# Optimization experiments

Hardware: AMD Instinct MI355X
Metric: run time of the kernel (lower is better)

The kernel has to match this reference:

```python
import jax, jax.numpy as jnp
import numpy as np


def _neighbor_sum(x_pad):
    """3x3 box filter with zero center (8-neighbor sum), VALID conv on a padded input."""
    k = jnp.array([[1., 1., 1.], [1., 0., 1.], [1., 1., 1.]], dtype=x_pad.dtype)
    k = k.reshape(1, 1, 3, 3)  # OIHW
    return jax.lax.conv_general_dilated(
        x_pad, k, window_strides=(1, 1), padding='VALID',
        dimension_numbers=('NCHW', 'OIHW', 'NCHW'))


def setup_inputs() -> dict:
    key = jax.random.key(0)
    k1, k2 = jax.random.split(key)
    B, C, H, W = 1, 1, 4096, 4096
    out_image = jax.random.uniform(k1, (B, C, H, W), dtype=jnp.float32)      # predicted probabilities
    segment_image = jax.random.uniform(k2, (B, C, H, W), dtype=jnp.float32)  # target map
    return {"out_image": out_image, "segment_image": segment_image}


def reference(out_image, segment_image):
    pad = ((0, 0), (0, 0), (1, 1), (1, 1))
    out_pad = jnp.pad(out_image, pad)          # constant 0 pad, as F.pad(..., value=0)
    seg_pad = jnp.pad(segment_image, pad)
    out_rev_pad = 1.0 - out_pad                # reverse AFTER padding: border becomes 1

    sig_seg_1 = 9.0 - _neighbor_sum(seg_pad)       # [B,C,H,W]
    sig_out_0 = 9.0 - _neighbor_sum(out_rev_pad)   # [B,C,H,W]

    W1 = jnp.squeeze(sig_seg_1)   # [H,W] for B=C=1
    M0 = jnp.squeeze(sig_out_0)
    seg = jnp.squeeze(segment_image)
    out = jnp.squeeze(out_image)

    eps = 1e-5
    loss = -(W1 * seg * jnp.log(out + eps) + M0 * (1.0 - seg) * jnp.log(1.0 - out + eps))
    return loss.mean()
```

## Files before the change

kernel.cpp:

```cpp
#include <hip/hip_runtime.h>

#define H 4096
#define W 4096
#define R 8
#define TC 4
#define TPB 256
#define STRIP (TPB*TC)
#define NSTRIP (W/STRIP)
#define NBAND (H/R)
#define NBLK (NSTRIP*NBAND)
#define LN2 0.69314718055994531f

template<bool INTERIOR>
__device__ __forceinline__ float band_loss(const float* __restrict__ sp0,
                                           const float* __restrict__ op0,
                                           int r0, bool lv, bool rv) {
  float sa[TC], sb[TC], sc[TC];
  float oa[TC], ob[TC], oc[TC];
  float sLa, sLb, sLc, sRa, sRb, sRc;
  float oLa, oLb, oLc, oRa, oRb, oRc;

  const float* sp = sp0 - W;
  const float* op = op0 - W;

  auto loadrow = [&](bool valid, float* sv, float* ov,
                     float& sl, float& sr, float& ol, float& orr) {
    if (valid) {
      const float4 fs = *reinterpret_cast<const float4*>(sp);
      const float4 fo = *reinterpret_cast<const float4*>(op);
      sv[0] = fs.x; sv[1] = fs.y; sv[2] = fs.z; sv[3] = fs.w;
      ov[0] = fo.x; ov[1] = fo.y; ov[2] = fo.z; ov[3] = fo.w;
      sl  = lv ? sp[-1] : 0.f;
      ol  = lv ? op[-1] : 0.f;
      sr  = rv ? sp[TC] : 0.f;
      orr = rv ? op[TC] : 0.f;
    } else {
      sv[0] = sv[1] = sv[2] = sv[3] = 0.f;
      ov[0] = ov[1] = ov[2] = ov[3] = 0.f;
      sl = sr = ol = orr = 0.f;
    }
  };

  loadrow(INTERIOR || (r0 - 1 >= 0), sa, oa, sLa, sRa, oLa, oRa);
  sp += W; op += W;
  loadrow(true, sb, ob, sLb, sRb, oLb, oRb);

  float acc = 0.f;

  #pragma unroll
  for (int i = 0; i < R; ++i) {
    sp += W; op += W;
    loadrow(INTERIOR || (r0 + i + 1 < H), sc, oc, sLc, sRc, oLc, oRc);

    float cs[TC], co[TC];
    #pragma unroll
    for (int k = 0; k < TC; ++k) {
      cs[k] = sa[k] + sb[k] + sc[k];
      co[k] = oa[k] + ob[k] + oc[k];
    }
    const float csL = sLa + sLb + sLc;
    const float csR = sRa + sRb + sRc;
    const float coL = oLa + oLb + oLc;
    const float coR = oRa + oRb + oRc;

    #pragma unroll
    for (int k = 0; k < TC; ++k) {
      const float cl  = (k == 0)    ? csL : cs[k-1];
      const float cr  = (k == TC-1) ? csR : cs[k+1];
      const float nsS = cl + cs[k] + cr - sb[k];
      const float col = (k == 0)    ? coL : co[k-1];
      const float cor = (k == TC-1) ? coR : co[k+1];
      const float nsO = col + co[k] + cor - ob[k];
      const float w1 = 9.f - nsS;
      const float m0 = 1.f + nsO;
      const float s = sb[k], o = ob[k];
      acc += w1 * s * __log2f(o + 1e-5f) + m0 * (1.f - s) * __log2f(1.00001f - o);
    }

    #pragma unroll
    for (int k = 0; k < TC; ++k) {
      sa[k] = sb[k]; sb[k] = sc[k];
      oa[k] = ob[k]; ob[k] = oc[k];
    }
    sLa = sLb; sLb = sLc;  sRa = sRb; sRb = sRc;
    oLa = oLb; oLb = oLc;  oRa = oRb; oRb = oRc;
  }
  return acc;
}

__global__ __launch_bounds__(TPB)
void wbce_kernel(const float* __restrict__ outp, const float* __restrict__ segp,
                 float* __restrict__ partial) {
  const int t     = threadIdx.x;
  const int strip = blockIdx.x;
  const int band  = blockIdx.y;
  const int r0    = band * R;
  const int c0    = strip * STRIP + t * TC;
  const bool lv   = (c0 > 0);
  const bool rv   = (c0 + TC < W);

  const float* sp0 = segp + (size_t)r0 * W + c0;
  const float* op0 = outp + (size_t)r0 * W + c0;

  float acc;
  if (band > 0 && band < NBAND - 1) acc = band_loss<true >(sp0, op0, r0, lv, rv);
  else                              acc = band_loss<false>(sp0, op0, r0, lv, rv);

  #pragma unroll
  for (int off = 32; off > 0; off >>= 1) acc += __shfl_down(acc, off, 64);

  __shared__ float wsum[TPB / 64];
  if ((t & 63) == 0) wsum[t >> 6] = acc;
  __syncthreads();
  if (t == 0)
    partial[band * NSTRIP + strip] = wsum[0] + wsum[1] + wsum[2] + wsum[3];
}

__global__ __launch_bounds__(64)
void reduce_kernel(const float* __restrict__ partial, float* __restrict__ out) {
  const int t = threadIdx.x;
  float a = 0.f;
  #pragma unroll
  for (int i = 0; i < NBLK / (64 * 4); ++i) {
    const float4 v = reinterpret_cast<const float4*>(partial)[t + i * 64];
    a += v.x + v.y + v.z + v.w;
  }
  #pragma unroll
  for (int off = 32; off > 0; off >>= 1) a += __shfl_down(a, off, 64);
  if (t == 0)
    out[0] = a * (-LN2 / ((float)H * (float)W));
}

extern "C" void kernel_launch(void* const* d_in, const int* in_sizes, int n_in,
                              void* d_out, int out_size, void* d_ws, size_t ws_size,
                              hipStream_t stream) {
  const float* outp = (const float*)d_in[0];
  const float* segp = (const float*)d_in[1];
  float* part = (float*)d_ws;
  float* o = (float*)d_out;
  wbce_kernel<<<dim3(NSTRIP, NBAND), TPB, 0, stream>>>(outp, segp, part);
  reduce_kernel<<<1, 64, 0, stream>>>(part, o);
}
```

Measured before the change: 32.56 us.

## Stream interior rows through LDS via async global_load_lds with wave-shuffle halos

For interior bands, each wave prefetches upcoming rows into a small triple-buffered LDS ring using async global-to-LDS loads with explicit vmcnt waits. Horizontal neighbour column sums come from cross-lane shuffles, and only the two wave-edge lanes load the extra halo columns. This replaces the per-thread scalar left/right loads of the old path. Per-wave partials are written directly, which drops the block-level syncthreads, and the final reduce is widened to 256 threads. The hand-written vmcnt counts depend on exact instruction ordering, which is fragile and adds LDS traffic.

```diff
diff --git a/kernel.cpp b/kernel.cpp
--- a/kernel.cpp
+++ b/kernel.cpp
@@ -8,21 +8,24 @@
 #define STRIP (TPB*TC)
 #define NSTRIP (W/STRIP)
 #define NBAND (H/R)
-#define NBLK (NSTRIP*NBAND)
+#define NPART (NSTRIP*NBAND*4)
+#define NS 3
 #define LN2 0.69314718055994531f
 
-template<bool INTERIOR>
-__device__ __forceinline__ float band_loss(const float* __restrict__ sp0,
-                                           const float* __restrict__ op0,
-                                           int r0, bool lv, bool rv) {
+__device__ __forceinline__ void dma16(const float* g, float* l) {
+  __builtin_amdgcn_global_load_lds((const __attribute__((address_space(1))) void*)g,
+                                   (__attribute__((address_space(3))) void*)l, 16, 0, 0);
+}
+
+__device__ float band_loss_edge(const float* __restrict__ sp0,
+                                const float* __restrict__ op0,
+                                int r0, bool lv, bool rv) {
   float sa[TC], sb[TC], sc[TC];
   float oa[TC], ob[TC], oc[TC];
   float sLa, sLb, sLc, sRa, sRb, sRc;
   float oLa, oLb, oLc, oRa, oRb, oRc;
-
   const float* sp = sp0 - W;
   const float* op = op0 - W;
-
   auto loadrow = [&](bool valid, float* sv, float* ov,
                      float& sl, float& sr, float& ol, float& orr) {
     if (valid) {
@@ -30,39 +33,29 @@
       const float4 fo = *reinterpret_cast<const float4*>(op);
       sv[0] = fs.x; sv[1] = fs.y; sv[2] = fs.z; sv[3] = fs.w;
       ov[0] = fo.x; ov[1] = fo.y; ov[2] = fo.z; ov[3] = fo.w;
-      sl  = lv ? sp[-1] : 0.f;
-      ol  = lv ? op[-1] : 0.f;
-      sr  = rv ? sp[TC] : 0.f;
-      orr = rv ? op[TC] : 0.f;
+      sl  = lv ? sp[-1] : 0.f;  ol  = lv ? op[-1] : 0.f;
+      sr  = rv ? sp[TC] : 0.f;  orr = rv ? op[TC] : 0.f;
     } else {
-      sv[0] = sv[1] = sv[2] = sv[3] = 0.f;
-      ov[0] = ov[1] = ov[2] = ov[3] = 0.f;
+      sv[0]=sv[1]=sv[2]=sv[3]=0.f; ov[0]=ov[1]=ov[2]=ov[3]=0.f;
       sl = sr = ol = orr = 0.f;
     }
   };
-
-  loadrow(INTERIOR || (r0 - 1 >= 0), sa, oa, sLa, sRa, oLa, oRa);
+  loadrow(r0 - 1 >= 0, sa, oa, sLa, sRa, oLa, oRa);
   sp += W; op += W;
   loadrow(true, sb, ob, sLb, sRb, oLb, oRb);
-
   float acc = 0.f;
-
   #pragma unroll
   for (int i = 0; i < R; ++i) {
     sp += W; op += W;
-    loadrow(INTERIOR || (r0 + i + 1 < H), sc, oc, sLc, sRc, oLc, oRc);
-
+    loadrow(r0 + i + 1 < H, sc, oc, sLc, sRc, oLc, oRc);
     float cs[TC], co[TC];
     #pragma unroll
     for (int k = 0; k < TC; ++k) {
       cs[k] = sa[k] + sb[k] + sc[k];
       co[k] = oa[k] + ob[k] + oc[k];
     }
-    const float csL = sLa + sLb + sLc;
-    const float csR = sRa + sRb + sRc;
-    const float coL = oLa + oLb + oLc;
-    const float coR = oRa + oRb + oRc;
-
+    const float csL = sLa + sLb + sLc, csR = sRa + sRb + sRc;
+    const float coL = oLa + oLb + oLc, coR = oRa + oRb + oRc;
     #pragma unroll
     for (int k = 0; k < TC; ++k) {
       const float cl  = (k == 0)    ? csL : cs[k-1];
@@ -76,7 +69,6 @@
       const float s = sb[k], o = ob[k];
       acc += w1 * s * __log2f(o + 1e-5f) + m0 * (1.f - s) * __log2f(1.00001f - o);
     }
-
     #pragma unroll
     for (int k = 0; k < TC; ++k) {
       sa[k] = sb[k]; sb[k] = sc[k];
@@ -94,41 +86,125 @@
   const int t     = threadIdx.x;
   const int strip = blockIdx.x;
   const int band  = blockIdx.y;
+  const int w     = t >> 6;
+  const int lane  = t & 63;
   const int r0    = band * R;
-  const int c0    = strip * STRIP + t * TC;
-  const bool lv   = (c0 > 0);
-  const bool rv   = (c0 + TC < W);
-
-  const float* sp0 = segp + (size_t)r0 * W + c0;
-  const float* op0 = outp + (size_t)r0 * W + c0;
-
-  float acc;
-  if (band > 0 && band < NBAND - 1) acc = band_loss<true >(sp0, op0, r0, lv, rv);
-  else                              acc = band_loss<false>(sp0, op0, r0, lv, rv);
+  const int wc0   = strip * STRIP + w * 256;
+  const int c0    = wc0 + lane * TC;
+
+  __shared__ __align__(16) float lds[4][NS][2][256];
+
+  float acc = 0.f;
+
+  if (band > 0 && band < NBAND - 1) {
+    float* slab = &lds[w][0][0][0];
+
+    float eS[R+2], eO[R+2];
+    #pragma unroll
+    for (int j = 0; j < R+2; ++j) { eS[j] = 0.f; eO[j] = 0.f; }
+    const bool eAct = (lane == 0 && wc0 > 0) || (lane == 63 && wc0 + 256 < W);
+    const int  ecol = (lane == 0) ? (wc0 - 1) : (wc0 + 256);
+    if (eAct) {
+      const float* es = segp + (size_t)(r0 - 1) * W + ecol;
+      const float* eo = outp + (size_t)(r0 - 1) * W + ecol;
+      #pragma unroll
+      for (int j = 0; j < R+2; ++j) {
+        eS[j] = es[(size_t)j * W];
+        eO[j] = eo[(size_t)j * W];
+      }
+    }
+
+    const float* sg = segp + (size_t)(r0 - 1) * W + c0;
+    const float* og = outp + (size_t)(r0 - 1) * W + c0;
+    float4 s0 = *reinterpret_cast<const float4*>(sg);
+    float4 o0 = *reinterpret_cast<const float4*>(og);
+    float4 s1 = *reinterpret_cast<const float4*>(sg + W);
+    float4 o1 = *reinterpret_cast<const float4*>(og + W);
+
+    const float* sd = sg + 2 * (size_t)W;
+    const float* od = og + 2 * (size_t)W;
+    dma16(sd,     slab + (2 % NS) * 512);
+    dma16(od,     slab + (2 % NS) * 512 + 256);
+    dma16(sd + W, slab + (3 % NS) * 512);
+    dma16(od + W, slab + (3 % NS) * 512 + 256);
+    sd += 2 * (size_t)W; od += 2 * (size_t)W;
+
+    #pragma unroll
+    for (int i = 0; i < R; ++i) {
+      if (i + 4 <= R + 1) {
+        const int sl = (i + 4) % NS;
+        dma16(sd, slab + sl * 512);
+        dma16(od, slab + sl * 512 + 256);
+        sd += W; od += W;
+      }
+      if (i < R - 2)       asm volatile("s_waitcnt vmcnt(4)" ::: "memory");
+      else if (i == R - 2) asm volatile("s_waitcnt vmcnt(2)" ::: "memory");
+      else                 asm volatile("s_waitcnt vmcnt(0)" ::: "memory");
+
+      const int sl2 = (i + 2) % NS;
+      const float4 s2 = *reinterpret_cast<const float4*>(slab + sl2 * 512 +       lane * 4);
+      const float4 o2 = *reinterpret_cast<const float4*>(slab + sl2 * 512 + 256 + lane * 4);
+
+      float cs[TC], co[TC];
+      cs[0] = s0.x + s1.x + s2.x;  cs[1] = s0.y + s1.y + s2.y;
+      cs[2] = s0.z + s1.z + s2.z;  cs[3] = s0.w + s1.w + s2.w;
+      co[0] = o0.x + o1.x + o2.x;  co[1] = o0.y + o1.y + o2.y;
+      co[2] = o0.z + o1.z + o2.z;  co[3] = o0.w + o1.w + o2.w;
+
+      const float esum_s = eS[i] + eS[i+1] + eS[i+2];
+      const float esum_o = eO[i] + eO[i+1] + eO[i+2];
+      float csL = __shfl_up(cs[3], 1, 64);   if (lane == 0)  csL = esum_s;
+      float coL = __shfl_up(co[3], 1, 64);   if (lane == 0)  coL = esum_o;
+      float csR = __shfl_down(cs[0], 1, 64); if (lane == 63) csR = esum_s;
+      float coR = __shfl_down(co[0], 1, 64); if (lane == 63) coR = esum_o;
+
+      const float sb[TC] = { s1.x, s1.y, s1.z, s1.w };
+      const float ob[TC] = { o1.x, o1.y, o1.z, o1.w };
+      #pragma unroll
+      for (int k = 0; k < TC; ++k) {
+        const float cl  = (k == 0)    ? csL : cs[k-1];
+        const float cr  = (k == TC-1) ? csR : cs[k+1];
+        const float nsS = cl + cs[k] + cr - sb[k];
+        const float col = (k == 0)    ? coL : co[k-1];
+        const float cor = (k == TC-1) ? coR : co[k+1];
+        const float nsO = col + co[k] + cor - ob[k];
+        const float w1 = 9.f - nsS;
+        const float m0 = 1.f + nsO;
+        const float s = sb[k], o = ob[k];
+        acc += w1 * s * __log2f(o + 1e-5f) + m0 * (1.f - s) * __log2f(1.00001f - o);
+      }
+
+      s0 = s1; s1 = s2;  o0 = o1; o1 = o2;
+    }
+  } else {
+    const bool lv = (c0 > 0);
+    const bool rv = (c0 + TC < W);
+    acc = band_loss_edge(segp + (size_t)r0 * W + c0,
+                         outp + (size_t)r0 * W + c0, r0, lv, rv);
+  }
 
   #pragma unroll
   for (int off = 32; off > 0; off >>= 1) acc += __shfl_down(acc, off, 64);
-
-  __shared__ float wsum[TPB / 64];
-  if ((t & 63) == 0) wsum[t >> 6] = acc;
-  __syncthreads();
-  if (t == 0)
-    partial[band * NSTRIP + strip] = wsum[0] + wsum[1] + wsum[2] + wsum[3];
-}
-
-__global__ __launch_bounds__(64)
+  if (lane == 0)
+    partial[((band * NSTRIP + strip) << 2) + w] = acc;
+}
+
+__global__ __launch_bounds__(TPB)
 void reduce_kernel(const float* __restrict__ partial, float* __restrict__ out) {
   const int t = threadIdx.x;
   float a = 0.f;
   #pragma unroll
-  for (int i = 0; i < NBLK / (64 * 4); ++i) {
-    const float4 v = reinterpret_cast<const float4*>(partial)[t + i * 64];
+  for (int i = 0; i < NPART / (TPB * 4); ++i) {
+    const float4 v = reinterpret_cast<const float4*>(partial)[t + i * TPB];
     a += v.x + v.y + v.z + v.w;
   }
   #pragma unroll
   for (int off = 32; off > 0; off >>= 1) a += __shfl_down(a, off, 64);
+  __shared__ float ws[TPB / 64];
+  if ((t & 63) == 0) ws[t >> 6] = a;
+  __syncthreads();
   if (t == 0)
-    out[0] = a * (-LN2 / ((float)H * (float)W));
+    out[0] = (ws[0] + ws[1] + ws[2] + ws[3]) * (-LN2 / ((float)H * (float)W));
 }
 
 extern "C" void kernel_launch(void* const* d_in, const int* in_sizes, int n_in,
@@ -139,5 +215,5 @@
   float* part = (float*)d_ws;
   float* o = (float*)d_out;
   wbce_kernel<<<dim3(NSTRIP, NBAND), TPB, 0, stream>>>(outp, segp, part);
-  reduce_kernel<<<1, 64, 0, stream>>>(part, o);
-}
+  reduce_kernel<<<1, TPB, 0, stream>>>(part, o);
+}
```

Measured after the change: 35.60 us. 1.09x slower.
